# Kernel optimization log

Measured on AMD Instinct MI355X. Metric: run time of the kernel, lower is better.

Reference implementation:

```python
import jax, jax.numpy as jnp
import numpy as np

B, T, C = 2, 2048, 1024
H, HS, RD = 16, 64, 64
KV_R, Q_R = 256, 384


def _rope_tables(T, dim):
    # standard RoPE angle tables, shape [T, dim]
    half = dim // 2
    inv_freq = 1.0 / (10000.0 ** (np.arange(0, half, dtype=np.float32) / half))
    t = np.arange(T, dtype=np.float32)
    ang = np.outer(t, inv_freq)  # [T, half]
    ang = np.concatenate([ang, ang], axis=-1)  # [T, dim]
    return jnp.asarray(np.cos(ang)), jnp.asarray(np.sin(ang))


def setup_inputs() -> dict:
    key = jax.random.key(0)
    ks = jax.random.split(key, 8)
    cos, sin = _rope_tables(T, RD)
    s = lambda fan_in: 1.0 / np.sqrt(fan_in)
    return {
        "x": jax.random.normal(ks[0], (B, T, C), jnp.float32),
        "cos": cos,
        "sin": sin,
        "W_kv_down": jax.random.normal(ks[1], (C, KV_R), jnp.float32) * s(C),
        "W_kv_up": jax.random.normal(ks[2], (KV_R, H * HS), jnp.float32) * s(KV_R),
        "W_k_rope": jax.random.normal(ks[3], (KV_R, H * RD), jnp.float32) * s(KV_R),
        "W_q_down": jax.random.normal(ks[4], (C, Q_R), jnp.float32) * s(C),
        "W_q_up": jax.random.normal(ks[5], (Q_R, H * HS), jnp.float32) * s(Q_R),
        "W_q_rope": jax.random.normal(ks[6], (Q_R, H * RD), jnp.float32) * s(Q_R),
        "W_out": jax.random.normal(ks[7], (H * HS, C), jnp.float32) * s(H * HS),
    }


def _apply_rope(x, cos, sin):
    # x: [B,H,T,D]; cos/sin: [T,D] broadcast
    d = x.shape[-1]
    x1, x2 = x[..., : d // 2], x[..., d // 2 :]
    rotated = jnp.concatenate([-x2, x1], axis=-1)
    return x * cos + rotated * sin


def reference(x, cos, sin, W_kv_down, W_kv_up, W_k_rope, W_q_down, W_q_up, W_q_rope, W_out):
    Bx, Tx, Cx = x.shape
    to_heads = lambda z, d: jnp.swapaxes(z.reshape(Bx, Tx, H, d), 1, 2)  # [B,H,T,d]

    latent_kv = x @ W_kv_down                      # [B,T,KV_R]
    kv_up = latent_kv @ W_kv_up                    # [B,T,H*HS]
    v = to_heads(kv_up, HS)
    k_content = to_heads(kv_up, HS)                # same projection used for k and v
    k_rope = _apply_rope(to_heads(latent_kv @ W_k_rope, RD), cos[:Tx], sin[:Tx])

    latent_q = x @ W_q_down                        # [B,T,Q_R]
    q_content = to_heads(latent_q @ W_q_up, HS)
    q_rope = _apply_rope(to_heads(latent_q @ W_q_rope, RD), cos[:Tx], sin[:Tx])

    q = jnp.concatenate([q_content, q_rope], axis=-1)  # [B,H,T,HS+RD]
    k = jnp.concatenate([k_content, k_rope], axis=-1)

    att = jnp.einsum("bhqd,bhkd->bhqk", q, k) * (HS ** -0.5)
    causal = jnp.tril(jnp.ones((Tx, Tx), bool))
    att = jnp.where(causal, att, -jnp.inf)
    att = jax.nn.softmax(att, axis=-1)             # dropout is eval-mode identity
    y = jnp.einsum("bhqk,bhkd->bhqd", att, v)      # [B,H,T,HS]
    y = jnp.swapaxes(y, 1, 2).reshape(Bx, Tx, H * HS)
    return y @ W_out
```

## Files before the change

kernel.cpp:

```cpp
#include <hip/hip_runtime.h>
#include <stdint.h>

typedef unsigned short u16;
typedef __bf16 bf16x8 __attribute__((ext_vector_type(8)));
typedef float f32x4 __attribute__((ext_vector_type(4)));

#define B_ 2
#define T_ 2048

__device__ __forceinline__ u16 f2b(float f) {
  unsigned u = __float_as_uint(f);
  u += 0x7fffu + ((u >> 16) & 1u);
  return (u16)(u >> 16);
}
__device__ __forceinline__ float b2f(u16 v) {
  return __uint_as_float(((unsigned)v) << 16);
}
__device__ __forceinline__ unsigned cvt_pk(float lo, float hi) {
  unsigned r;
  asm("v_cvt_pk_bf16_f32 %0, %1, %2" : "=v"(r) : "v"(lo), "v"(hi));
  return r;
}
__device__ __forceinline__ float ex2(float x) {
  float r;
  asm("v_exp_f32 %0, %1" : "=v"(r) : "v"(x));
  return r;
}

using gu32 = __attribute__((address_space(1))) const unsigned int;
using lu32 = __attribute__((address_space(3))) unsigned int;
__device__ __forceinline__ void gl_lds16(const u16* g, u16* l) {
  __builtin_amdgcn_global_load_lds((gu32*)g, (lu32*)l, 16, 0, 0);
}

struct TJob { const float* src; u16* dst; int K, N, ldt, row_off, blk0; };
struct TJobs { TJob j[7]; };

__global__ __launch_bounds__(256) void prep_kernel(const float* __restrict__ x,
                                                   u16* __restrict__ xb, TJobs jobs) {
  int bid = blockIdx.x;
  int tid = threadIdx.x;
  if (bid < 4096) {
    int i = (bid * 256 + tid) * 4;
    float4 v = *reinterpret_cast<const float4*>(x + i);
    union { u16 h[4]; unsigned long long ll; } pk;
    pk.h[0] = f2b(v.x); pk.h[1] = f2b(v.y); pk.h[2] = f2b(v.z); pk.h[3] = f2b(v.w);
    *reinterpret_cast<unsigned long long*>(xb + i) = pk.ll;
    return;
  }
  bid -= 4096;
  __shared__ float tile[32][33];
  int ji = 0;
  #pragma unroll
  for (int i = 6; i > 0; --i)
    if (bid >= jobs.j[i].blk0) { ji = i; break; }
  const TJob jb = jobs.j[ji];
  int local = bid - jb.blk0;
  int nb = jb.N >> 5;
  int n0 = (local % nb) * 32, k0 = (local / nb) * 32;
  int cx = tid & 31, ry = tid >> 5;
  #pragma unroll
  for (int i = 0; i < 4; i++)
    tile[ry + i * 8][cx] = jb.src[(size_t)(k0 + ry + i * 8) * jb.N + n0 + cx];
  __syncthreads();
  #pragma unroll
  for (int i = 0; i < 4; i++)
    jb.dst[(size_t)(jb.row_off + n0 + ry + i * 8) * jb.ldt + k0 + cx] =
        f2b(tile[cx][ry + i * 8]);
}

struct GJob { const u16* A; const u16* Bt; void* C; int lda, ldb, ldc, K, mode; };

__global__ __launch_bounds__(512) void gemm_bt8(GJob j0, GJob j1, int split,
                                                u16* __restrict__ vt,
                                                const float* __restrict__ cosT,
                                                const float* __restrict__ sinT) {
  __shared__ u16 As[2][128 * 32];
  __shared__ u16 Bs[2][128 * 32];
  const bool first = (int)blockIdx.x < split;
  const GJob jb = first ? j0 : j1;
  const int bx = blockIdx.x - (first ? 0 : split);
  const int tid = threadIdx.x;
  const int wave = tid >> 6, lane = tid & 63;
  const int wr = wave >> 1, wc = wave & 1;
  const int l15 = lane & 15, l4 = lane >> 4;
  const int m0 = blockIdx.y * 128, n0 = bx * 128;
  const int lr = lane >> 2;
  const int lc = (lane & 3) * 8;

  f32x4 acc[2][4];
  const f32x4 fzero = {0.f, 0.f, 0.f, 0.f};
  #pragma unroll
  for (int m = 0; m < 2; m++)
    #pragma unroll
    for (int n = 0; n < 4; n++)
      acc[m][n] = fzero;

  const u16* gA = jb.A  + (size_t)(m0 + wave * 16 + lr) * jb.lda + lc;
  const u16* gB = jb.Bt + (size_t)(n0 + wave * 16 + lr) * jb.ldb + lc;

  auto stage = [&](int buf, int k0) {
    gl_lds16(gA + k0, &As[buf][(wave * 16) * 32]);
    gl_lds16(gB + k0, &Bs[buf][(wave * 16) * 32]);
  };

  stage(0, 0);
  int buf = 0;
  const int K = jb.K;
  for (int k0 = 0; k0 < K; k0 += 32) {
    asm volatile("s_waitcnt vmcnt(0)" ::: "memory");
    __builtin_amdgcn_s_barrier();
    if (k0 + 32 < K) stage(buf ^ 1, k0 + 32);
    bf16x8 af[2], bfr[4];
    #pragma unroll
    for (int m = 0; m < 2; m++)
      af[m] = *reinterpret_cast<const bf16x8*>(&As[buf][(wr * 32 + m * 16 + l15) * 32 + l4 * 8]);
    #pragma unroll
    for (int n = 0; n < 4; n++)
      bfr[n] = *reinterpret_cast<const bf16x8*>(&Bs[buf][(wc * 64 + n * 16 + l15) * 32 + l4 * 8]);
    #pragma unroll
    for (int m = 0; m < 2; m++)
      #pragma unroll
      for (int n = 0; n < 4; n++)
        acc[m][n] = __builtin_amdgcn_mfma_f32_16x16x32_bf16(af[m], bfr[n], acc[m][n], 0, 0, 0);
    buf ^= 1;
  }

  const int row_base = m0 + wr * 32 + l4 * 4;
  const int col_base = n0 + wc * 64 + l15;
  const int mode = jb.mode;
  const int ldc = jb.ldc;

  if (mode == 1) {
    float* Cf = (float*)jb.C;
    #pragma unroll
    for (int m = 0; m < 2; m++)
      #pragma unroll
      for (int n = 0; n < 4; n++)
        #pragma unroll
        for (int r = 0; r < 4; r++)
          Cf[(size_t)(row_base + m * 16 + r) * ldc + col_base + n * 16] = acc[m][n][r];
    return;
  }

  if (mode >= 2 && (n0 + wc * 64) >= 1024) {
    #pragma unroll
    for (int m = 0; m < 2; m++)
      #pragma unroll
      for (int r = 0; r < 4; r++) {
        int t = (row_base + m * 16 + r) & (T_ - 1);
        const float* cp = cosT + t * 64 + l15;
        const float* sp = sinT + t * 64 + l15;
        float c0 = cp[0], c16 = cp[16], c32 = cp[32], c48 = cp[48];
        float s0 = sp[0], s16 = sp[16], s32 = sp[32], s48 = sp[48];
        float x0 = acc[m][0][r], x1 = acc[m][1][r];
        float x2 = acc[m][2][r], x3 = acc[m][3][r];
        acc[m][0][r] = x0 * c0 - x2 * s0;
        acc[m][1][r] = x1 * c16 - x3 * s16;
        acc[m][2][r] = x2 * c32 + x0 * s32;
        acc[m][3][r] = x3 * c48 + x1 * s48;
      }
  }

  u16* Cb = (u16*)jb.C;
  #pragma unroll
  for (int m = 0; m < 2; m++)
    #pragma unroll
    for (int n = 0; n < 4; n++)
      #pragma unroll
      for (int r = 0; r < 4; r++)
        Cb[(size_t)(row_base + m * 16 + r) * ldc + col_base + n * 16] = f2b(acc[m][n][r]);

  if (mode == 2) {
    #pragma unroll
    for (int m = 0; m < 2; m++)
      #pragma unroll
      for (int n = 0; n < 4; n++) {
        int col = col_base + n * 16;
        if (col < 1024) {
          int mm = row_base + m * 16;
          int bb = mm >> 11, tt = mm & 2047;
          uint2 pk2;
          pk2.x = cvt_pk(acc[m][n][0], acc[m][n][1]);
          pk2.y = cvt_pk(acc[m][n][2], acc[m][n][3]);
          *reinterpret_cast<uint2*>(&vt[(size_t)(bb * 1024 + col) * 2048 + tt]) = pk2;
        }
      }
  }
}

__global__ __launch_bounds__(512) void attn_kernel(const u16* __restrict__ qo,
                                                   const u16* __restrict__ kvo,
                                                   const u16* __restrict__ vtg,
                                                   u16* __restrict__ yb) {
  __shared__ u16 K_lds[2][64 * 128];
  __shared__ u16 V_lds[2][64 * 64];
  __shared__ u16 P_lds[8][16][72];
  const int tid = threadIdx.x;
  const int wave = tid >> 6, lane = tid & 63;
  const int l15 = lane & 15, l4 = lane >> 4;
  const int bid = blockIdx.x;
  const int bh = bid & 31;
  const int qi = 15 - (bid >> 5);
  const int b = bh >> 4, h = bh & 15;
  const int q0 = qi * 128;
  const int qrow = q0 + wave * 16 + l15;

  const u16* qb = qo + (size_t)(b * T_ + qrow) * 2048 + h * 64;
  bf16x8 qf[4];
  qf[0] = *reinterpret_cast<const bf16x8*>(qb + l4 * 8);
  qf[1] = *reinterpret_cast<const bf16x8*>(qb + 32 + l4 * 8);
  qf[2] = *reinterpret_cast<const bf16x8*>(qb + 1024 + l4 * 8);
  qf[3] = *reinterpret_cast<const bf16x8*>(qb + 1056 + l4 * 8);

  const u16* Kbase = kvo + (size_t)(b * T_) * 2048 + h * 64;
  const u16* Vbase = vtg + (size_t)(b * 1024 + h * 64) * 2048;

  const int krow_i = lane >> 4;
  const int kc2 = (lane & 15) * 16;
  const int vrow_i = lane >> 3;
  const int vc2 = (lane & 7) * 16;

  auto stage = [&](int buf, int kv0) {
    #pragma unroll
    for (int j = 0; j < 2; j++) {
      int row = wave * 8 + j * 4 + krow_i;
      int c2x = kc2 ^ ((row & 7) << 4);
      int cu = c2x >> 1;
      const u16* src = Kbase + (size_t)(kv0 + row) * 2048 + (cu < 64 ? cu : 960 + cu);
      gl_lds16(src, &K_lds[buf][(wave * 8 + j * 4) * 128]);
    }
    {
      int row = wave * 8 + vrow_i;
      int c2x = vc2 ^ ((row & 7) << 4);
      const u16* src = Vbase + (size_t)row * 2048 + kv0 + (c2x >> 1);
      gl_lds16(src, &V_lds[buf][(wave * 8) * 64]);
    }
  };

  const f32x4 fzero = {0.f, 0.f, 0.f, 0.f};
  f32x4 oT[4];
  #pragma unroll
  for (int f = 0; f < 4; f++) oT[f] = fzero;
  float m_run = -1e30f, l_run = 0.f;

  const float SCALE2 = 0.125f * 1.44269504f;
  const int nt = qi * 2 + 2;
  const int t_diag = qi * 2 + (wave >> 2);

  stage(0, 0);
  int buf = 0;

  for (int t = 0; t < nt; t++) {
    const int kv0 = t * 64;
    asm volatile("s_waitcnt vmcnt(0)" ::: "memory");
    __builtin_amdgcn_s_barrier();
    if (t + 1 < nt) stage(buf ^ 1, kv0 + 64);

    if (t <= t_diag) {
      const char* Kb = (const char*)&K_lds[buf][0];
      const char* Vb = (const char*)&V_lds[buf][0];

      f32x4 sT[4];
      #pragma unroll
      for (int c = 0; c < 4; c++) sT[c] = fzero;
      #pragma unroll
      for (int c = 0; c < 4; c++) {
        const int krow = c * 16 + l15;
        const int kxm = (krow & 7) << 4;
        #pragma unroll
        for (int s = 0; s < 4; s++) {
          bf16x8 kf = *reinterpret_cast<const bf16x8*>(
              Kb + krow * 256 + ((s * 64 + l4 * 16) ^ kxm));
          sT[c] = __builtin_amdgcn_mfma_f32_16x16x32_bf16(kf, qf[s], sT[c], 0, 0, 0);
        }
      }

      const bool diag = (t == t_diag);
      float p[4][4];
      float mx = -1e30f;
      #pragma unroll
      for (int c = 0; c < 4; c++)
        #pragma unroll
        for (int r = 0; r < 4; r++) {
          float s = sT[c][r] * SCALE2;
          if (diag) {
            int kv = kv0 + c * 16 + l4 * 4 + r;
            if (kv > qrow) s = -1e30f;
          }
          p[c][r] = s;
          mx = fmaxf(mx, s);
        }
      mx = fmaxf(mx, __shfl_xor(mx, 16));
      mx = fmaxf(mx, __shfl_xor(mx, 32));
      if (__any(mx > m_run + 11.5f)) {
        float m_new = fmaxf(m_run, mx);
        float corr = ex2(m_run - m_new);
        l_run *= corr;
        #pragma unroll
        for (int f = 0; f < 4; f++) oT[f] *= corr;
        m_run = m_new;
      }
      float rsum = 0.f;
      #pragma unroll
      for (int c = 0; c < 4; c++)
        #pragma unroll
        for (int r = 0; r < 4; r++) {
          float pe = ex2(p[c][r] - m_run);
          p[c][r] = pe;
          rsum += pe;
        }
      rsum += __shfl_xor(rsum, 16);
      rsum += __shfl_xor(rsum, 32);
      l_run += rsum;

      #pragma unroll
      for (int c = 0; c < 4; c++) {
        uint2 pk2;
        pk2.x = cvt_pk(p[c][0], p[c][1]);
        pk2.y = cvt_pk(p[c][2], p[c][3]);
        *reinterpret_cast<uint2*>(&P_lds[wave][l15][c * 16 + l4 * 4]) = pk2;
      }
      bf16x8 pb0 = *reinterpret_cast<const bf16x8*>(&P_lds[wave][l15][l4 * 8]);
      bf16x8 pb1 = *reinterpret_cast<const bf16x8*>(&P_lds[wave][l15][32 + l4 * 8]);

      #pragma unroll
      for (int f = 0; f < 4; f++) {
        const int vrow = f * 16 + l15;
        const int vxm = (vrow & 7) << 4;
        bf16x8 v0 = *reinterpret_cast<const bf16x8*>(Vb + vrow * 128 + ((l4 * 16) ^ vxm));
        bf16x8 v1 = *reinterpret_cast<const bf16x8*>(Vb + vrow * 128 + ((64 + l4 * 16) ^ vxm));
        oT[f] = __builtin_amdgcn_mfma_f32_16x16x32_bf16(v0, pb0, oT[f], 0, 0, 0);
        oT[f] = __builtin_amdgcn_mfma_f32_16x16x32_bf16(v1, pb1, oT[f], 0, 0, 0);
      }
    }

    buf ^= 1;
  }

  const float inv = 1.f / l_run;
  #pragma unroll
  for (int f = 0; f < 4; f++) {
    uint2 pk2;
    pk2.x = cvt_pk(oT[f][0] * inv, oT[f][1] * inv);
    pk2.y = cvt_pk(oT[f][2] * inv, oT[f][3] * inv);
    *reinterpret_cast<uint2*>(
        &yb[(size_t)(b * T_ + qrow) * 1024 + h * 64 + f * 16 + l4 * 4]) = pk2;
  }
}

extern "C" void kernel_launch(void* const* d_in, const int* in_sizes, int n_in,
                              void* d_out, int out_size, void* d_ws, size_t ws_size,
                              hipStream_t stream) {
  const float* x         = (const float*)d_in[0];
  const float* cosT      = (const float*)d_in[1];
  const float* sinT      = (const float*)d_in[2];
  const float* W_kv_down = (const float*)d_in[3];
  const float* W_kv_up   = (const float*)d_in[4];
  const float* W_k_rope  = (const float*)d_in[5];
  const float* W_q_down  = (const float*)d_in[6];
  const float* W_q_up    = (const float*)d_in[7];
  const float* W_q_rope  = (const float*)d_in[8];
  const float* W_out     = (const float*)d_in[9];
  float* out = (float*)d_out;
  char* ws = (char*)d_ws;

  u16* xb    = (u16*)(ws + 0);
  u16* lat   = (u16*)(ws + 8388608);
  u16* WdT   = (u16*)(ws + 13631488);
  u16* WkvT  = (u16*)(ws + 14942208);
  u16* WqT   = (u16*)(ws + 15990784);
  u16* WoutT = (u16*)(ws + 17563648);
  u16* kvo   = (u16*)(ws + 19660800);
  u16* qo    = (u16*)(ws + 36438016);
  u16* VT    = (u16*)(ws + 53215232);
  u16* yb    = (u16*)(ws + 0);

  TJobs jobs;
  jobs.j[0] = {W_kv_down, WdT,   1024, 256,  1024, 0,    0};
  jobs.j[1] = {W_q_down,  WdT,   1024, 384,  1024, 256,  256};
  jobs.j[2] = {W_kv_up,   WkvT,  256,  1024, 256,  0,    640};
  jobs.j[3] = {W_k_rope,  WkvT,  256,  1024, 256,  1024, 896};
  jobs.j[4] = {W_q_up,    WqT,   384,  1024, 384,  0,    1152};
  jobs.j[5] = {W_q_rope,  WqT,   384,  1024, 384,  1024, 1536};
  jobs.j[6] = {W_out,     WoutT, 1024, 1024, 1024, 0,    1920};
  prep_kernel<<<7040, 256, 0, stream>>>(x, xb, jobs);

  GJob g1 = {xb, WdT, lat, 1024, 1024, 640, 1024, 0};
  gemm_bt8<<<dim3(5, 32), 512, 0, stream>>>(g1, g1, 5, nullptr, nullptr, nullptr);

  GJob g2 = {lat,       WkvT, kvo, 640, 256, 2048, 256, 2};
  GJob g3 = {lat + 256, WqT,  qo,  640, 384, 2048, 384, 3};
  gemm_bt8<<<dim3(32, 32), 512, 0, stream>>>(g2, g3, 16, VT, cosT, sinT);

  attn_kernel<<<512, 512, 0, stream>>>(qo, kvo, VT, yb);

  GJob g4 = {yb, WoutT, out, 1024, 1024, 1024, 1024, 1};
  gemm_bt8<<<dim3(8, 32), 512, 0, stream>>>(g4, g4, 8, nullptr, nullptr, nullptr);
}
```

Measured before the change: 220.1 us.

## Double GEMM K-tile to 64 with XOR-swizzled LDS, move V transpose to separate kernel

The GEMM now stages 64-wide K tiles into LDS using an XOR swizzle on the column index, which halves the number of barriers per K and is meant to avoid LDS bank conflicts on fragment reads. The strided transposed V store is removed from the up-projection epilogue. A dedicated tiled transpose kernel now builds VT from kvo. This adds an extra kernel launch and an extra read and write of V, and doubles the GEMM's LDS use, which may lower occupancy.

Result: faster. 215.7 us (-2.0%).

```diff
diff --git a/kernel.cpp b/kernel.cpp
--- a/kernel.cpp
+++ b/kernel.cpp
@@ -12,9 +12,6 @@
   unsigned u = __float_as_uint(f);
   u += 0x7fffu + ((u >> 16) & 1u);
   return (u16)(u >> 16);
-}
-__device__ __forceinline__ float b2f(u16 v) {
-  return __uint_as_float(((unsigned)v) << 16);
 }
 __device__ __forceinline__ unsigned cvt_pk(float lo, float hi) {
   unsigned r;
@@ -72,11 +69,10 @@
 struct GJob { const u16* A; const u16* Bt; void* C; int lda, ldb, ldc, K, mode; };
 
 __global__ __launch_bounds__(512) void gemm_bt8(GJob j0, GJob j1, int split,
-                                                u16* __restrict__ vt,
                                                 const float* __restrict__ cosT,
                                                 const float* __restrict__ sinT) {
-  __shared__ u16 As[2][128 * 32];
-  __shared__ u16 Bs[2][128 * 32];
+  __shared__ u16 As[2][128 * 64];
+  __shared__ u16 Bs[2][128 * 64];
   const bool first = (int)blockIdx.x < split;
   const GJob jb = first ? j0 : j1;
   const int bx = blockIdx.x - (first ? 0 : split);
@@ -85,8 +81,8 @@
   const int wr = wave >> 1, wc = wave & 1;
   const int l15 = lane & 15, l4 = lane >> 4;
   const int m0 = blockIdx.y * 128, n0 = bx * 128;
-  const int lr = lane >> 2;
-  const int lc = (lane & 3) * 8;
+  const int srow = lane >> 3;
+  const int scol = ((lane & 7) ^ srow) * 8;
 
   f32x4 acc[2][4];
   const f32x4 fzero = {0.f, 0.f, 0.f, 0.f};
@@ -96,33 +92,45 @@
     for (int n = 0; n < 4; n++)
       acc[m][n] = fzero;
 
-  const u16* gA = jb.A  + (size_t)(m0 + wave * 16 + lr) * jb.lda + lc;
-  const u16* gB = jb.Bt + (size_t)(n0 + wave * 16 + lr) * jb.ldb + lc;
+  const u16* gA = jb.A  + (size_t)(m0 + wave * 16 + srow) * jb.lda + scol;
+  const u16* gB = jb.Bt + (size_t)(n0 + wave * 16 + srow) * jb.ldb + scol;
 
   auto stage = [&](int buf, int k0) {
-    gl_lds16(gA + k0, &As[buf][(wave * 16) * 32]);
-    gl_lds16(gB + k0, &Bs[buf][(wave * 16) * 32]);
+    gl_lds16(gA + k0,                      &As[buf][(wave * 16) * 64]);
+    gl_lds16(gA + (size_t)8 * jb.lda + k0, &As[buf][(wave * 16 + 8) * 64]);
+    gl_lds16(gB + k0,                      &Bs[buf][(wave * 16) * 64]);
+    gl_lds16(gB + (size_t)8 * jb.ldb + k0, &Bs[buf][(wave * 16 + 8) * 64]);
   };
 
   stage(0, 0);
   int buf = 0;
   const int K = jb.K;
-  for (int k0 = 0; k0 < K; k0 += 32) {
+  for (int k0 = 0; k0 < K; k0 += 64) {
     asm volatile("s_waitcnt vmcnt(0)" ::: "memory");
     __builtin_amdgcn_s_barrier();
-    if (k0 + 32 < K) stage(buf ^ 1, k0 + 32);
-    bf16x8 af[2], bfr[4];
+    if (k0 + 64 < K) stage(buf ^ 1, k0 + 64);
+    bf16x8 af[2][2], bfr[4][2];
+    #pragma unroll
+    for (int m = 0; m < 2; m++) {
+      const int row = wr * 32 + m * 16 + l15;
+      const int xm = (row & 7) * 8;
+      af[m][0] = *reinterpret_cast<const bf16x8*>(&As[buf][row * 64 + ((l4 * 8) ^ xm)]);
+      af[m][1] = *reinterpret_cast<const bf16x8*>(&As[buf][row * 64 + ((32 + l4 * 8) ^ xm)]);
+    }
+    #pragma unroll
+    for (int n = 0; n < 4; n++) {
+      const int row = wc * 64 + n * 16 + l15;
+      const int xm = (row & 7) * 8;
+      bfr[n][0] = *reinterpret_cast<const bf16x8*>(&Bs[buf][row * 64 + ((l4 * 8) ^ xm)]);
+      bfr[n][1] = *reinterpret_cast<const bf16x8*>(&Bs[buf][row * 64 + ((32 + l4 * 8) ^ xm)]);
+    }
     #pragma unroll
     for (int m = 0; m < 2; m++)
-      af[m] = *reinterpret_cast<const bf16x8*>(&As[buf][(wr * 32 + m * 16 + l15) * 32 + l4 * 8]);
-    #pragma unroll
-    for (int n = 0; n < 4; n++)
-      bfr[n] = *reinterpret_cast<const bf16x8*>(&Bs[buf][(wc * 64 + n * 16 + l15) * 32 + l4 * 8]);
-    #pragma unroll
-    for (int m = 0; m < 2; m++)
-      #pragma unroll
-      for (int n = 0; n < 4; n++)
-        acc[m][n] = __builtin_amdgcn_mfma_f32_16x16x32_bf16(af[m], bfr[n], acc[m][n], 0, 0, 0);
+      #pragma unroll
+      for (int n = 0; n < 4; n++) {
+        acc[m][n] = __builtin_amdgcn_mfma_f32_16x16x32_bf16(af[m][0], bfr[n][0], acc[m][n], 0, 0, 0);
+        acc[m][n] = __builtin_amdgcn_mfma_f32_16x16x32_bf16(af[m][1], bfr[n][1], acc[m][n], 0, 0, 0);
+      }
     buf ^= 1;
   }
 
@@ -170,22 +178,32 @@
       #pragma unroll
       for (int r = 0; r < 4; r++)
         Cb[(size_t)(row_base + m * 16 + r) * ldc + col_base + n * 16] = f2b(acc[m][n][r]);
-
-  if (mode == 2) {
-    #pragma unroll
-    for (int m = 0; m < 2; m++)
-      #pragma unroll
-      for (int n = 0; n < 4; n++) {
-        int col = col_base + n * 16;
-        if (col < 1024) {
-          int mm = row_base + m * 16;
-          int bb = mm >> 11, tt = mm & 2047;
-          uint2 pk2;
-          pk2.x = cvt_pk(acc[m][n][0], acc[m][n][1]);
-          pk2.y = cvt_pk(acc[m][n][2], acc[m][n][3]);
-          *reinterpret_cast<uint2*>(&vt[(size_t)(bb * 1024 + col) * 2048 + tt]) = pk2;
-        }
-      }
+}
+
+__global__ __launch_bounds__(256) void vtrans_kernel(const u16* __restrict__ kvo,
+                                                     u16* __restrict__ vt) {
+  __shared__ u16 tile[64][72];
+  const int tid = threadIdx.x;
+  const int cb = blockIdx.x * 64;
+  const int rb = blockIdx.y * 64;
+  const int b = rb >> 11, t0 = rb & 2047;
+  const int rr = tid >> 3;
+  const int c8 = (tid & 7) * 8;
+  #pragma unroll
+  for (int i = 0; i < 2; i++) {
+    int r = i * 32 + rr;
+    uint4 v = *reinterpret_cast<const uint4*>(kvo + (size_t)(rb + r) * 2048 + cb + c8);
+    *reinterpret_cast<uint4*>(&tile[r][c8]) = v;
+  }
+  __syncthreads();
+  #pragma unroll
+  for (int i = 0; i < 2; i++) {
+    int c = i * 32 + rr;
+    int r8 = c8;
+    union { u16 h[8]; uint4 v; } pk;
+    #pragma unroll
+    for (int j = 0; j < 8; j++) pk.h[j] = tile[r8 + j][c];
+    *reinterpret_cast<uint4*>(&vt[(size_t)(b * 1024 + cb + c) * 2048 + t0 + r8]) = pk.v;
   }
 }
 
@@ -387,14 +405,16 @@
   prep_kernel<<<7040, 256, 0, stream>>>(x, xb, jobs);
 
   GJob g1 = {xb, WdT, lat, 1024, 1024, 640, 1024, 0};
-  gemm_bt8<<<dim3(5, 32), 512, 0, stream>>>(g1, g1, 5, nullptr, nullptr, nullptr);
+  gemm_bt8<<<dim3(5, 32), 512, 0, stream>>>(g1, g1, 5, nullptr, nullptr);
 
   GJob g2 = {lat,       WkvT, kvo, 640, 256, 2048, 256, 2};
   GJob g3 = {lat + 256, WqT,  qo,  640, 384, 2048, 384, 3};
-  gemm_bt8<<<dim3(32, 32), 512, 0, stream>>>(g2, g3, 16, VT, cosT, sinT);
+  gemm_bt8<<<dim3(32, 32), 512, 0, stream>>>(g2, g3, 16, cosT, sinT);
+
+  vtrans_kernel<<<dim3(16, 64), 256, 0, stream>>>(kvo, VT);
 
   attn_kernel<<<512, 512, 0, stream>>>(qo, kvo, VT, yb);
 
   GJob g4 = {yb, WoutT, out, 1024, 1024, 1024, 1024, 1};
-  gemm_bt8<<<dim3(8, 32), 512, 0, stream>>>(g4, g4, 8, nullptr, nullptr, nullptr);
-}
+  gemm_bt8<<<dim3(8, 32), 512, 0, stream>>>(g4, g4, 8, nullptr, nullptr);
+}
```
